# Kernel tuning notes

Measured on AMD Instinct MI355X. Metric: run time of the kernel, lower is better.

Reference implementation:

```python
import jax, jax.numpy as jnp
import numpy as np

B, NB, T, C, H = 4, 256, 33, 512, 8
HD = C // H
SCALE = HD ** -0.5


def setup_inputs() -> dict:
    key = jax.random.key(0)
    ks = jax.random.split(key, 8)
    x = jax.random.normal(ks[0], (B, NB * T, C), jnp.float32)
    m = jax.random.randint(ks[1], (NB, T, T), 0, 2)
    eye = jnp.eye(T, dtype=m.dtype)
    attn_mask = jnp.maximum(m, eye[None, :, :]).astype(jnp.int32)  # diag always attendable
    edge_feats = jax.random.normal(ks[2], (NB, T, T, 4), jnp.float32)
    Wqkv = jax.random.normal(ks[3], (3 * C, C), jnp.float32) * (C ** -0.5)
    bqkv = jnp.zeros((3 * C,), jnp.float32)
    Wproj = jax.random.normal(ks[4], (C, C), jnp.float32) * (C ** -0.5)
    bproj = jnp.zeros((C,), jnp.float32)
    Wgate = jax.random.normal(ks[5], (H, 4), jnp.float32) * 0.01  # init.normal_(std=0.01)
    bgate = jnp.zeros((H,), jnp.float32)
    return dict(x=x, attn_mask=attn_mask, edge_feats=edge_feats,
                Wqkv=Wqkv, bqkv=bqkv, Wproj=Wproj, bproj=bproj,
                Wgate=Wgate, bgate=bgate)


def reference(x, attn_mask, edge_feats, Wqkv, bqkv, Wproj, bproj, Wgate, bgate):
    Bq, N, Cd = x.shape
    x_blk = x.reshape(Bq, NB, T, Cd)                         # (B,nb,T,C)
    qkv = x_blk @ Wqkv.T + bqkv                              # (B,nb,T,3C)
    q, k, v = jnp.split(qkv, 3, axis=-1)
    q = q.reshape(Bq, NB, T, H, HD)
    k = k.reshape(Bq, NB, T, H, HD)
    v = v.reshape(Bq, NB, T, H, HD)
    scores = jnp.einsum('bnqhd,bnkhd->bnqkh', q, k) * SCALE  # (B,nb,T,T,H)

    # physics bias: copy edge_feats[...,:4], overwrite diagonal to (0,0,0,1)
    bias = jnp.broadcast_to(edge_feats[None, ..., :4], (Bq, NB, T, T, 4))
    eye = jnp.eye(T, dtype=bool)[None, None, :, :, None]
    diag_vals = jnp.array([0.0, 0.0, 0.0, 1.0], dtype=bias.dtype)
    bias = jnp.where(eye, diag_vals, bias)

    scores = scores + bias[..., 3:4]                         # broadcast over heads
    mask_e = (attn_mask[None, :, :, :, None] != 0)           # (1,nb,T,T,1)
    scores = jnp.where(mask_e, scores, -jnp.inf)
    probs = jax.nn.softmax(scores, axis=3)                   # softmax over keys

    gates = bias @ Wgate.T + bgate                           # (B,nb,T,T,H)
    gates = jnp.where(mask_e, gates, 0.0)
    cw = probs + gates                                       # combined weights

    out = jnp.einsum('bnqkh,bnkhd->bnqhd', cw, v).reshape(Bq, NB, T, Cd)
    out = out @ Wproj.T + bproj
    return out.reshape(Bq, NB * T, Cd)
```

## Files before the change

### kernel.cpp

```cpp
#include <hip/hip_runtime.h>

typedef _Float16 half8 __attribute__((ext_vector_type(8)));
typedef _Float16 half4v __attribute__((ext_vector_type(4)));
typedef float floatx4 __attribute__((ext_vector_type(4)));
typedef unsigned uint4v __attribute__((ext_vector_type(4)));
typedef unsigned uint2v __attribute__((ext_vector_type(2)));

#define KDIM 512

__device__ __forceinline__ void gll16(const _Float16* g, void* l) {
  __builtin_amdgcn_global_load_lds((const __attribute__((address_space(1))) void*)g,
                                   (__attribute__((address_space(3))) void*)l, 16, 0, 0);
}

__device__ __forceinline__ unsigned pack2(float a, float b) {
  return __builtin_bit_cast(unsigned, __builtin_amdgcn_cvt_pkrtz(a, b));
}

__global__ void cvt_w(const float* __restrict__ wq, const float* __restrict__ wp,
                      _Float16* __restrict__ wqh, _Float16* __restrict__ wph) {
  long stride = (long)gridDim.x * blockDim.x;
  long t0 = (long)blockIdx.x * blockDim.x + threadIdx.x;
  for (long i = t0; i < 786432L/4; i += stride) {
    float4 v = ((const float4*)wq)[i];
    half4v h; h[0]=(_Float16)v.x; h[1]=(_Float16)v.y; h[2]=(_Float16)v.z; h[3]=(_Float16)v.w;
    ((half4v*)wqh)[i] = h;
  }
  for (long i = t0; i < 262144L/4; i += stride) {
    float4 v = ((const float4*)wp)[i];
    half4v h; h[0]=(_Float16)v.x; h[1]=(_Float16)v.y; h[2]=(_Float16)v.z; h[3]=(_Float16)v.w;
    ((half4v*)wph)[i] = h;
  }
}

__global__ __launch_bounds__(256, 2) void gemm1_f32a(const float* __restrict__ X,
    const _Float16* __restrict__ Bw, const float* __restrict__ bias,
    _Float16* __restrict__ Cout) {
  __shared__ __attribute__((aligned(16))) _Float16 As[128 * 64];
  __shared__ __attribute__((aligned(16))) _Float16 Bs[128 * 64];
  const int NN = 1536, ntile = 12;
  int bid = blockIdx.x;
  int xcd = bid & 7, idx = bid >> 3;
  int mt = (idx / ntile) * 8 + xcd;
  int nt = idx % ntile;
  long arow0 = (long)mt * 128;
  int bcol0 = nt * 128;
  int tid = threadIdx.x;
  int lane = tid & 63, w = tid >> 6;
  int wr = w >> 1, wc = w & 1;
  int g = lane >> 4, c = lane & 15;
  int wbase = tid & ~63;

  float4 ra[4][2];
  auto LOADA = [&](int kt) {
#pragma unroll
    for (int j = 0; j < 4; ++j) {
      int id4 = j * 256 + tid;
      int row = id4 >> 3, s = id4 & 7;
      const float* p = X + (arow0 + row) * 512L + kt * 64 + s * 8;
      ra[j][0] = *(const float4*)p;
      ra[j][1] = *(const float4*)(p + 4);
    }
  };
  auto WRITEA = [&]() {
#pragma unroll
    for (int j = 0; j < 4; ++j) {
      int id4 = j * 256 + tid;
      int row = id4 >> 3, s = id4 & 7;
      half8 h;
      h[0]=(_Float16)ra[j][0].x; h[1]=(_Float16)ra[j][0].y;
      h[2]=(_Float16)ra[j][0].z; h[3]=(_Float16)ra[j][0].w;
      h[4]=(_Float16)ra[j][1].x; h[5]=(_Float16)ra[j][1].y;
      h[6]=(_Float16)ra[j][1].z; h[7]=(_Float16)ra[j][1].w;
      *(half8*)((char*)As + row * 128 + ((s ^ (row & 7)) << 4)) = h;
    }
  };
  auto STAGEB = [&](int kt) {
#pragma unroll
    for (int j = 0; j < 4; ++j) {
      int id4 = j * 256 + tid;
      int row = id4 >> 3;
      int sc = (id4 & 7) ^ (row & 7);
      gll16(Bw + ((long)(bcol0 + row) * 512 + kt * 64 + sc * 8),
            (char*)Bs + (j * 256 + wbase) * 16);
    }
  };

  floatx4 acc[4][4];
#pragma unroll
  for (int i = 0; i < 4; i++)
#pragma unroll
    for (int j = 0; j < 4; j++) acc[i][j] = (floatx4)0.0f;

  LOADA(0);
  for (int kt = 0; kt < 8; ++kt) {
    if (kt) __syncthreads();
    WRITEA();
    STAGEB(kt);
    __syncthreads();
    if (kt < 7) LOADA(kt + 1);
#pragma unroll
    for (int ks = 0; ks < 2; ++ks) {
      half8 af[4], bf[4];
      int cb = ks * 64 + g * 16;
#pragma unroll
      for (int i = 0; i < 4; ++i) {
        int ra_ = wr * 64 + i * 16 + c;
        af[i] = *(const half8*)((const char*)As + ra_ * 128 + (cb ^ ((ra_ & 7) << 4)));
        int rb = wc * 64 + i * 16 + c;
        bf[i] = *(const half8*)((const char*)Bs + rb * 128 + (cb ^ ((rb & 7) << 4)));
      }
#pragma unroll
      for (int mi = 0; mi < 4; mi++)
#pragma unroll
        for (int ni = 0; ni < 4; ni++)
          acc[mi][ni] = __builtin_amdgcn_mfma_f32_16x16x32_f16(af[mi], bf[ni], acc[mi][ni], 0, 0, 0);
    }
  }
  long crow0 = arow0 + wr * 64;
  int ccol0 = bcol0 + wc * 64;
#pragma unroll
  for (int mi = 0; mi < 4; mi++)
#pragma unroll
    for (int ni = 0; ni < 4; ni++) {
      int col = ccol0 + ni * 16 + c;
      float bv = bias[col];
#pragma unroll
      for (int j = 0; j < 4; j++) {
        long r = crow0 + mi * 16 + g * 4 + j;
        Cout[r * NN + col] = (_Float16)(acc[mi][ni][j] + bv);
      }
    }
}

template<int NN, bool OUTF16>
__global__ __launch_bounds__(256, 2) void gemm_bt(const _Float16* __restrict__ A,
    const _Float16* __restrict__ Bw, const float* __restrict__ bias,
    void* __restrict__ Cout) {
  __shared__ __attribute__((aligned(16))) _Float16 As[128*64];
  __shared__ __attribute__((aligned(16))) _Float16 Bs[128*64];
  const int ntile = NN / 128;
  int bid = blockIdx.x;
  int xcd = bid & 7, idx = bid >> 3;
  int mt = (idx / ntile) * 8 + xcd;
  int nt = idx % ntile;
  int tid = threadIdx.x;
  int lane = tid & 63;
  int w = tid >> 6, wr = w >> 1, wc = w & 1;
  int g = lane >> 4, c = lane & 15;
  long arow0 = (long)mt * 128;
  int bcol0 = nt * 128;
  floatx4 acc[4][4];
#pragma unroll
  for (int i = 0; i < 4; i++)
#pragma unroll
    for (int j = 0; j < 4; j++) acc[i][j] = (floatx4)0.0f;

  int wbase = tid & ~63;
  for (int kt = 0; kt < KDIM / 64; ++kt) {
    if (kt) __syncthreads();
    int k0 = kt * 64;
#pragma unroll
    for (int j = 0; j < 4; ++j) {
      int idx4 = j * 256 + tid;
      int row = idx4 >> 3;
      int sc = (idx4 & 7) ^ (row & 7);
      gll16(A + ((arow0 + row) * KDIM + k0 + sc * 8), (char*)As + (j * 256 + wbase) * 16);
      gll16(Bw + ((long)(bcol0 + row) * KDIM + k0 + sc * 8), (char*)Bs + (j * 256 + wbase) * 16);
    }
    __syncthreads();
#pragma unroll
    for (int ks = 0; ks < 2; ++ks) {
      half8 af[4], bf[4];
      int cb = ks * 64 + g * 16;
#pragma unroll
      for (int i = 0; i < 4; ++i) {
        int ra = wr * 64 + i * 16 + c;
        af[i] = *(const half8*)((const char*)As + ra * 128 + (cb ^ ((ra & 7) << 4)));
        int rb = wc * 64 + i * 16 + c;
        bf[i] = *(const half8*)((const char*)Bs + rb * 128 + (cb ^ ((rb & 7) << 4)));
      }
#pragma unroll
      for (int mi = 0; mi < 4; mi++)
#pragma unroll
        for (int ni = 0; ni < 4; ni++)
          acc[mi][ni] = __builtin_amdgcn_mfma_f32_16x16x32_f16(af[mi], bf[ni], acc[mi][ni], 0, 0, 0);
    }
  }
  long crow0 = arow0 + wr * 64;
  int ccol0 = bcol0 + wc * 64;
#pragma unroll
  for (int mi = 0; mi < 4; mi++) {
#pragma unroll
    for (int ni = 0; ni < 4; ni++) {
      int col = ccol0 + ni * 16 + c;
      float bv = bias[col];
#pragma unroll
      for (int j = 0; j < 4; j++) {
        long r = crow0 + mi * 16 + g * 4 + j;
        float v = acc[mi][ni][j] + bv;
        if (OUTF16) ((_Float16*)Cout)[r * NN + col] = (_Float16)v;
        else        ((float*)Cout)[r * NN + col] = v;
      }
    }
  }
}

__global__ __launch_bounds__(256, 4) void attn_mid(const _Float16* __restrict__ qkv,
    const int* __restrict__ amask, const float* __restrict__ ef,
    const float* __restrict__ Wg, const float* __restrict__ bg,
    _Float16* __restrict__ aout) {
  __shared__ __attribute__((aligned(16))) half4v efT[48][42];
  __shared__ __attribute__((aligned(16))) _Float16 outb[4][33][88];
  __shared__ unsigned long long mrow[48];
  int blk = blockIdx.x;
  int nb = blk & 255;
  long R0 = (long)blk * 33;
  int tid = threadIdx.x;
  int lane = tid & 63, w = tid >> 6;
  int g = lane >> 4, c = lane & 15;

  if (tid < 48) {
    unsigned long long bits = 0;
    if (tid < 33) {
      const int* mp = amask + ((long)nb * 33 + tid) * 33;
      for (int k = 0; k < 33; k++) if (mp[k]) bits |= (1ull << k);
    }
    mrow[tid] = bits;
  }
  for (int u = tid; u < 48 * 42; u += 256) {
    int k = u / 42, q = u - k * 42;
    half4v hv; hv[0] = (_Float16)0.f; hv[1] = (_Float16)0.f; hv[2] = (_Float16)0.f; hv[3] = (_Float16)0.f;
    if (q < 33 && k < 33) {
      if (q == k) hv[3] = (_Float16)1.0f;
      else {
        float4 e4 = *(const float4*)(ef + (((long)nb * 33 + q) * 33 + k) * 4);
        hv[0] = (_Float16)e4.x; hv[1] = (_Float16)e4.y; hv[2] = (_Float16)e4.z; hv[3] = (_Float16)e4.w;
      }
    }
    efT[k][q] = hv;
  }
  __syncthreads();

  for (int hh = 0; hh < 2; ++hh) {
    int h = w + 4 * hh;
    float wg0 = Wg[h * 4 + 0], wg1 = Wg[h * 4 + 1], wg2 = Wg[h * 4 + 2], wg3 = Wg[h * 4 + 3];
    float bgh = bg[h];
    half8 qf[3][2], kf[3][2];
#pragma unroll
    for (int t3 = 0; t3 < 3; ++t3) {
      int t = t3 * 16 + c;
      long tr = R0 + (t < 33 ? t : 0);
#pragma unroll
      for (int ks = 0; ks < 2; ++ks) {
        int d0 = ks * 32 + g * 8;
        qf[t3][ks] = *(const half8*)(qkv + tr * 1536 + h * 64 + d0);
        kf[t3][ks] = *(const half8*)(qkv + tr * 1536 + 512 + h * 64 + d0);
      }
    }
    floatx4 s[3][3];
#pragma unroll
    for (int kt = 0; kt < 3; kt++)
#pragma unroll
      for (int qt = 0; qt < 3; qt++) s[kt][qt] = (floatx4)0.0f;
#pragma unroll
    for (int ks = 0; ks < 2; ++ks)
#pragma unroll
      for (int kt = 0; kt < 3; kt++)
#pragma unroll
        for (int qt = 0; qt < 3; qt++)
          s[kt][qt] = __builtin_amdgcn_mfma_f32_16x16x32_f16(kf[kt][ks], qf[qt][ks], s[kt][qt], 0, 0, 0);

    unsigned pk[2][3][2];
    float cw32[3];
#pragma unroll
    for (int qt = 0; qt < 3; qt++) {
      int q = qt * 16 + c;
      unsigned long long mb = mrow[q];
      float sv[3][4];
#pragma unroll
      for (int kt = 0; kt < 3; kt++)
#pragma unroll
        for (int j = 0; j < 4; j++) {
          int k = kt * 16 + 4 * g + j;
          float e3 = (float)efT[k][q][3];
          bool mk = (mb >> k) & 1;
          sv[kt][j] = mk ? s[kt][qt][j] * 0.125f + e3 : -1e30f;
        }
      float m = sv[0][0];
#pragma unroll
      for (int kt = 0; kt < 3; kt++)
#pragma unroll
        for (int j = 0; j < 4; j++) m = fmaxf(m, sv[kt][j]);
      m = fmaxf(m, __shfl_xor(m, 16, 64));
      m = fmaxf(m, __shfl_xor(m, 32, 64));
      float p[3][4], sum = 0.f;
#pragma unroll
      for (int kt = 0; kt < 3; kt++)
#pragma unroll
        for (int j = 0; j < 4; j++) { p[kt][j] = __expf(sv[kt][j] - m); sum += p[kt][j]; }
      sum += __shfl_xor(sum, 16, 64);
      sum += __shfl_xor(sum, 32, 64);
      float inv = __builtin_amdgcn_rcpf(sum);
      float cw[3][4];
#pragma unroll
      for (int kt = 0; kt < 3; kt++)
#pragma unroll
        for (int j = 0; j < 4; j++) {
          int k = kt * 16 + 4 * g + j;
          bool mk = (mb >> k) & 1;
          half4v e = efT[k][q];
          float gate = (float)e[0] * wg0 + (float)e[1] * wg1 + (float)e[2] * wg2 + (float)e[3] * wg3 + bgh;
          cw[kt][j] = mk ? p[kt][j] * inv + gate : 0.0f;
        }
#pragma unroll
      for (int kt = 0; kt < 2; kt++)
#pragma unroll
        for (int jp = 0; jp < 2; jp++) pk[kt][qt][jp] = pack2(cw[kt][2 * jp], cw[kt][2 * jp + 1]);
      cw32[qt] = cw[2][0];
    }

    half8 pb[3];
#pragma unroll
    for (int qt = 0; qt < 3; qt++) {
      uint4v d;
#pragma unroll
      for (int w2 = 0; w2 < 4; w2++) {
        int srcl = (((g & 1) * 2 + (w2 >> 1)) << 4) | c;
        unsigned v0 = (unsigned)__shfl((int)pk[0][qt][w2 & 1], srcl, 64);
        unsigned v1 = (unsigned)__shfl((int)pk[1][qt][w2 & 1], srcl, 64);
        d[w2] = (g >> 1) ? v1 : v0;
      }
      pb[qt] = __builtin_bit_cast(half8, d);
    }

    floatx4 o[4][3];
#pragma unroll
    for (int dt = 0; dt < 4; dt++)
#pragma unroll
      for (int qt = 0; qt < 3; qt++) o[dt][qt] = (floatx4)0.0f;
#pragma unroll
    for (int dh = 0; dh < 2; dh++) {
      half8 vf[2];
#pragma unroll
      for (int di = 0; di < 2; di++) {
        int dt = dh * 2 + di;
        half8 v;
#pragma unroll
        for (int e = 0; e < 8; e++)
          v[e] = qkv[(R0 + g * 8 + e) * 1536 + 1024 + h * 64 + dt * 16 + c];
        vf[di] = v;
      }
#pragma unroll
      for (int di = 0; di < 2; di++)
#pragma unroll
        for (int qt = 0; qt < 3; qt++)
          o[dh * 2 + di][qt] = __builtin_amdgcn_mfma_f32_16x16x32_f16(vf[di], pb[qt], o[dh * 2 + di][qt], 0, 0, 0);
    }
    float p32[3];
#pragma unroll
    for (int qt = 0; qt < 3; qt++) p32[qt] = __shfl(cw32[qt], c, 64);
#pragma unroll
    for (int dt = 0; dt < 4; dt++) {
      half4v v32 = *(const half4v*)(qkv + (R0 + 32) * 1536 + 1024 + h * 64 + dt * 16 + 4 * g);
#pragma unroll
      for (int qt = 0; qt < 3; qt++)
#pragma unroll
        for (int j = 0; j < 4; j++) o[dt][qt][j] += (float)v32[j] * p32[qt];
    }

#pragma unroll
    for (int qt = 0; qt < 3; qt++) {
      int q = qt * 16 + c;
      if (q < 33) {
#pragma unroll
        for (int dt = 0; dt < 4; dt++) {
          uint2v uu;
          uu[0] = pack2(o[dt][qt][0], o[dt][qt][1]);
          uu[1] = pack2(o[dt][qt][2], o[dt][qt][3]);
          *(uint2v*)&outb[w][q][dt * 16 + 4 * g] = uu;
        }
      }
    }
#pragma unroll
    for (int r0 = 0; r0 < 5; ++r0) {
      int q = r0 * 8 + (lane >> 3);
      if (q < 33) {
        half8 vv = *(const half8*)&outb[w][q][(lane & 7) * 8];
        *(half8*)(aout + (R0 + q) * 512 + h * 64 + (lane & 7) * 8) = vv;
      }
    }
  }
}

extern "C" void kernel_launch(void* const* d_in, const int* in_sizes, int n_in,
                              void* d_out, int out_size, void* d_ws, size_t ws_size,
                              hipStream_t stream) {
  const float* x  = (const float*)d_in[0];
  const int*   am = (const int*)d_in[1];
  const float* ef = (const float*)d_in[2];
  const float* Wq = (const float*)d_in[3];
  const float* bq = (const float*)d_in[4];
  const float* Wp = (const float*)d_in[5];
  const float* bp = (const float*)d_in[6];
  const float* Wg = (const float*)d_in[7];
  const float* bg = (const float*)d_in[8];
  char* ws = (char*)d_ws;
  _Float16* wqh  = (_Float16*)(ws);
  _Float16* wph  = (_Float16*)(ws + 2097152L);
  _Float16* qkv  = (_Float16*)(ws + 4194304L);
  _Float16* aout = (_Float16*)(ws + 108003328L);

  hipLaunchKernelGGL(cvt_w, dim3(512), dim3(256), 0, stream, Wq, Wp, wqh, wph);
  hipLaunchKernelGGL(gemm1_f32a, dim3(3168), dim3(256), 0, stream, x, wqh, bq, qkv);
  hipLaunchKernelGGL(attn_mid, dim3(1024), dim3(256), 0, stream, qkv, am, ef, Wg, bg, aout);
  hipLaunchKernelGGL((gemm_bt<512, false>), dim3(1056), dim3(256), 0, stream, aout, wph, bp, (float*)d_out);
}
```

Baseline: 152.9 us.

## Stage fp32 X directly into LDS via global_load_lds and convert at fragment load

The QKV GEMM now copies the fp32 activation tile straight into shared memory with asynchronous global-to-LDS loads and converts to fp16 when building MFMA fragments. This replaces the earlier register prefetch plus convert-and-store staging. It removes per-thread register staging and allows a higher occupancy target (3 blocks per CU). The cost is a doubled A tile in LDS (32KB fp32), twice the LDS read traffic, and conversions repeated per warp. It also loses the software prefetch overlap of the next tile's global load with compute. The weight-conversion grid is also halved.

```diff
diff --git a/kernel.cpp b/kernel.cpp
--- a/kernel.cpp
+++ b/kernel.cpp
@@ -8,7 +8,7 @@
 
 #define KDIM 512
 
-__device__ __forceinline__ void gll16(const _Float16* g, void* l) {
+__device__ __forceinline__ void gll16(const void* g, void* l) {
   __builtin_amdgcn_global_load_lds((const __attribute__((address_space(1))) void*)g,
                                    (__attribute__((address_space(3))) void*)l, 16, 0, 0);
 }
@@ -33,10 +33,10 @@
   }
 }
 
-__global__ __launch_bounds__(256, 2) void gemm1_f32a(const float* __restrict__ X,
+__global__ __launch_bounds__(256, 3) void gemm1_xf32(const float* __restrict__ X,
     const _Float16* __restrict__ Bw, const float* __restrict__ bias,
     _Float16* __restrict__ Cout) {
-  __shared__ __attribute__((aligned(16))) _Float16 As[128 * 64];
+  __shared__ __attribute__((aligned(16))) float    Af[128 * 64];
   __shared__ __attribute__((aligned(16))) _Float16 Bs[128 * 64];
   const int NN = 1536, ntile = 12;
   int bid = blockIdx.x;
@@ -51,64 +51,50 @@
   int g = lane >> 4, c = lane & 15;
   int wbase = tid & ~63;
 
-  float4 ra[4][2];
-  auto LOADA = [&](int kt) {
-#pragma unroll
-    for (int j = 0; j < 4; ++j) {
-      int id4 = j * 256 + tid;
-      int row = id4 >> 3, s = id4 & 7;
-      const float* p = X + (arow0 + row) * 512L + kt * 64 + s * 8;
-      ra[j][0] = *(const float4*)p;
-      ra[j][1] = *(const float4*)(p + 4);
-    }
-  };
-  auto WRITEA = [&]() {
-#pragma unroll
-    for (int j = 0; j < 4; ++j) {
-      int id4 = j * 256 + tid;
-      int row = id4 >> 3, s = id4 & 7;
-      half8 h;
-      h[0]=(_Float16)ra[j][0].x; h[1]=(_Float16)ra[j][0].y;
-      h[2]=(_Float16)ra[j][0].z; h[3]=(_Float16)ra[j][0].w;
-      h[4]=(_Float16)ra[j][1].x; h[5]=(_Float16)ra[j][1].y;
-      h[6]=(_Float16)ra[j][1].z; h[7]=(_Float16)ra[j][1].w;
-      *(half8*)((char*)As + row * 128 + ((s ^ (row & 7)) << 4)) = h;
-    }
-  };
-  auto STAGEB = [&](int kt) {
-#pragma unroll
-    for (int j = 0; j < 4; ++j) {
-      int id4 = j * 256 + tid;
+  floatx4 acc[4][4];
+#pragma unroll
+  for (int i = 0; i < 4; i++)
+#pragma unroll
+    for (int j = 0; j < 4; j++) acc[i][j] = (floatx4)0.0f;
+
+  for (int kt = 0; kt < 8; ++kt) {
+    if (kt) __syncthreads();
+    int k0 = kt * 64;
+#pragma unroll
+    for (int u = 0; u < 8; ++u) {
+      int id4 = u * 256 + tid;
+      int row = id4 >> 4;
+      int sc = (id4 & 15) ^ (row & 7);
+      gll16(X + (arow0 + row) * 512L + k0 + sc * 4,
+            (char*)Af + (u * 256 + wbase) * 16);
+    }
+#pragma unroll
+    for (int u = 0; u < 4; ++u) {
+      int id4 = u * 256 + tid;
       int row = id4 >> 3;
       int sc = (id4 & 7) ^ (row & 7);
-      gll16(Bw + ((long)(bcol0 + row) * 512 + kt * 64 + sc * 8),
-            (char*)Bs + (j * 256 + wbase) * 16);
-    }
-  };
-
-  floatx4 acc[4][4];
-#pragma unroll
-  for (int i = 0; i < 4; i++)
-#pragma unroll
-    for (int j = 0; j < 4; j++) acc[i][j] = (floatx4)0.0f;
-
-  LOADA(0);
-  for (int kt = 0; kt < 8; ++kt) {
-    if (kt) __syncthreads();
-    WRITEA();
-    STAGEB(kt);
+      gll16(Bw + ((long)(bcol0 + row) * 512 + k0 + sc * 8),
+            (char*)Bs + (u * 256 + wbase) * 16);
+    }
     __syncthreads();
-    if (kt < 7) LOADA(kt + 1);
 #pragma unroll
     for (int ks = 0; ks < 2; ++ks) {
       half8 af[4], bf[4];
-      int cb = ks * 64 + g * 16;
 #pragma unroll
       for (int i = 0; i < 4; ++i) {
-        int ra_ = wr * 64 + i * 16 + c;
-        af[i] = *(const half8*)((const char*)As + ra_ * 128 + (cb ^ ((ra_ & 7) << 4)));
+        int ra = wr * 64 + i * 16 + c;
+        const char* abase = (const char*)Af + ra * 256;
+        int x7a = (ra & 7) << 4;
+        int cba = ks * 128 + g * 32;
+        float4 f0 = *(const float4*)(abase + ((cba) ^ x7a));
+        float4 f1 = *(const float4*)(abase + ((cba + 16) ^ x7a));
+        half8 h;
+        h[0]=(_Float16)f0.x; h[1]=(_Float16)f0.y; h[2]=(_Float16)f0.z; h[3]=(_Float16)f0.w;
+        h[4]=(_Float16)f1.x; h[5]=(_Float16)f1.y; h[6]=(_Float16)f1.z; h[7]=(_Float16)f1.w;
+        af[i] = h;
         int rb = wc * 64 + i * 16 + c;
-        bf[i] = *(const half8*)((const char*)Bs + rb * 128 + (cb ^ ((rb & 7) << 4)));
+        int cbb = ks * 64 + g * 16;
+        bf[i] = *(const half8*)((const char*)Bs + rb * 128 + (cbb ^ ((rb & 7) << 4)));
       }
 #pragma unroll
       for (int mi = 0; mi < 4; mi++)
@@ -411,8 +397,8 @@
   _Float16* qkv  = (_Float16*)(ws + 4194304L);
   _Float16* aout = (_Float16*)(ws + 108003328L);
 
-  hipLaunchKernelGGL(cvt_w, dim3(512), dim3(256), 0, stream, Wq, Wp, wqh, wph);
-  hipLaunchKernelGGL(gemm1_f32a, dim3(3168), dim3(256), 0, stream, x, wqh, bq, qkv);
+  hipLaunchKernelGGL(cvt_w, dim3(256), dim3(256), 0, stream, Wq, Wp, wqh, wph);
+  hipLaunchKernelGGL(gemm1_xf32, dim3(3168), dim3(256), 0, stream, x, wqh, bq, qkv);
   hipLaunchKernelGGL(attn_mid, dim3(1024), dim3(256), 0, stream, qkv, am, ef, Wg, bg, aout);
   hipLaunchKernelGGL((gemm_bt<512, false>), dim3(1056), dim3(256), 0, stream, aout, wph, bp, (float*)d_out);
 }
```

New measurement: 160.0 us. 4.7% more time.
